# Optimization experiments

Hardware: AMD Instinct MI355X
Metric: run time of the kernel (lower is better)

## Reference

```python
import jax, jax.numpy as jnp
import numpy as np

EPS = 0.97  # ContrastLoss eps
T = 0.07    # temperature

def _embed(x, W, b):
    # Linear + L2 normalize (Normalize(power=2))
    h = x @ W.T + b                     # [B, feat_dim]
    norm = jnp.sqrt(jnp.sum(h * h, axis=1, keepdims=True))
    return h / norm

def setup_inputs() -> dict:
    key = jax.random.key(0)
    ks = jax.random.split(key, 7)
    B, S, Td, F = 8192, 2048, 2048, 128
    return {
        "f_s": jax.random.normal(ks[0], (B, S), jnp.float32),
        "f_t": jax.random.normal(ks[1], (B, Td), jnp.float32),
        "y": jax.random.randint(ks[2], (B,), 0, 100, jnp.int64),
        "W_s": jax.random.normal(ks[3], (F, S), jnp.float32) * 0.02,
        "b_s": jax.random.normal(ks[4], (F,), jnp.float32) * 0.02,
        "W_t": jax.random.normal(ks[5], (F, Td), jnp.float32) * 0.02,
        "b_t": jax.random.normal(ks[6], (F,), jnp.float32) * 0.02,
    }

def reference(f_s, f_t, y, W_s, b_s, W_t, b_t):
    fs = _embed(f_s, W_s, b_s)
    ft = _embed(f_t, W_t, b_t)
    # CRDLoss re-normalizes (idempotent, kept for fidelity)
    fs = fs / jnp.linalg.norm(fs, axis=1, keepdims=True)
    ft = ft / jnp.linalg.norm(ft, axis=1, keepdims=True)
    bsz = fs.shape[0]
    x = jnp.exp((fs @ ft.T) / T)  # [B, B] exponentiated similarities
    same = y[None, :] == y[:, None]        # y_expand == y_expand.T
    diag = jnp.eye(bsz, dtype=bool)
    pos_mask = same & ~diag
    neg_mask = ~same & ~diag
    # masked log-ratio sums instead of dynamic-shape gathers
    log_D1 = jnp.log(x / (x + EPS))
    log_D0 = jnp.log(EPS / (x + EPS))
    loss = -(jnp.sum(jnp.where(pos_mask, log_D1, 0.0))
             + jnp.sum(jnp.where(neg_mask, log_D0, 0.0))) / bsz
    return loss
```

## Files before the change

### kernel.cpp

```cpp
#include <hip/hip_runtime.h>
#include <math.h>


typedef _Float16 half_t;
typedef half_t halfx4 __attribute__((ext_vector_type(4)));
typedef half_t halfx8 __attribute__((ext_vector_type(8)));
typedef float f32x4 __attribute__((ext_vector_type(4)));

#define B_TOT   8192
#define K_EMB   2048
#define F_DIM   128
#define INV_T   14.285714285714286f
#define EPS_C   0.97f
#define LOG_EPS (-0.030459207485f)

__global__ __launch_bounds__(256) void cvt_w_kernel(
    const float* __restrict__ Ws, const float* __restrict__ Wt,
    half_t* __restrict__ Ws16, half_t* __restrict__ Wt16)
{
    const float* src = blockIdx.y ? Wt : Ws;
    half_t* dst = blockIdx.y ? Wt16 : Ws16;
    int pos4 = blockIdx.x * 256 + threadIdx.x;
    float4 v = *(const float4*)(src + (size_t)pos4 * 4);
    halfx4 h4 = {(half_t)v.x, (half_t)v.y, (half_t)v.z, (half_t)v.w};
    *(halfx4*)(dst + (size_t)pos4 * 4) = h4;
}

__global__ __launch_bounds__(256) void embed_kernel(
    const float* __restrict__ Xs, const float* __restrict__ Xt,
    const half_t* __restrict__ Ws16, const half_t* __restrict__ Wt16,
    const float* __restrict__ bs, const float* __restrict__ bt,
    half_t* __restrict__ outs, half_t* __restrict__ outt)
{
    const float* X; const half_t* W16; const float* bias; half_t* out;
    if (blockIdx.y == 0) { X = Xs; W16 = Ws16; bias = bs; out = outs; }
    else                 { X = Xt; W16 = Wt16; bias = bt; out = outt; }

    __shared__ half_t As[2][32][72];
    __shared__ half_t Bs[2][128][72];
    __shared__ float  biasS[128];
    __shared__ float  redS[32][2];
    __shared__ float  invS[32];

    const int tid = threadIdx.x;
    const int r0  = blockIdx.x * 32;
    if (tid < 128) biasS[tid] = bias[tid];

    const int lane = tid & 63;
    const int w    = tid >> 6;
    const int wm   = w & 1, wn = w >> 1;
    const int l16  = lane & 15, lhi = lane >> 4;

    f32x4 acc[4];
    for (int in = 0; in < 4; ++in) acc[in] = f32x4{0.f, 0.f, 0.f, 0.f};

    const int ar0 = tid >> 4, ar1 = (tid + 256) >> 4;
    const int akq = (tid & 15) * 4;
    const int bc  = (tid & 7) * 8;

    float4 na[2]; uint4 nb[4];

    na[0] = *(const float4*)(X + (size_t)(r0 + ar0) * K_EMB + akq);
    na[1] = *(const float4*)(X + (size_t)(r0 + ar1) * K_EMB + akq);
#pragma unroll
    for (int i = 0; i < 4; ++i)
        nb[i] = *(const uint4*)(W16 + (size_t)((tid + i * 256) >> 3) * K_EMB + bc);
    {
        halfx4 h0 = {(half_t)na[0].x, (half_t)na[0].y, (half_t)na[0].z, (half_t)na[0].w};
        halfx4 h1 = {(half_t)na[1].x, (half_t)na[1].y, (half_t)na[1].z, (half_t)na[1].w};
        *(halfx4*)&As[0][ar0][akq] = h0;
        *(halfx4*)&As[0][ar1][akq] = h1;
#pragma unroll
        for (int i = 0; i < 4; ++i)
            *(uint4*)&Bs[0][(tid + i * 256) >> 3][bc] = nb[i];
    }
    __syncthreads();

    for (int it = 0; it < 32; ++it) {
        const int cur = it & 1;
        if (it < 31) {
            const int kb = (it + 1) * 64;
            na[0] = *(const float4*)(X + (size_t)(r0 + ar0) * K_EMB + kb + akq);
            na[1] = *(const float4*)(X + (size_t)(r0 + ar1) * K_EMB + kb + akq);
#pragma unroll
            for (int i = 0; i < 4; ++i)
                nb[i] = *(const uint4*)(W16 + (size_t)((tid + i * 256) >> 3) * K_EMB + kb + bc);
        }
#pragma unroll
        for (int kk = 0; kk < 2; ++kk) {
            halfx8 a, b[4];
            a = *(const halfx8*)&As[cur][wm * 16 + l16][kk * 32 + lhi * 8];
#pragma unroll
            for (int in = 0; in < 4; ++in)
                b[in] = *(const halfx8*)&Bs[cur][wn * 64 + in * 16 + l16][kk * 32 + lhi * 8];
#pragma unroll
            for (int in = 0; in < 4; ++in)
                acc[in] = __builtin_amdgcn_mfma_f32_16x16x32_f16(a, b[in], acc[in], 0, 0, 0);
        }
        if (it < 31) {
            const int nxt = cur ^ 1;
            halfx4 h0 = {(half_t)na[0].x, (half_t)na[0].y, (half_t)na[0].z, (half_t)na[0].w};
            halfx4 h1 = {(half_t)na[1].x, (half_t)na[1].y, (half_t)na[1].z, (half_t)na[1].w};
            *(halfx4*)&As[nxt][ar0][akq] = h0;
            *(halfx4*)&As[nxt][ar1][akq] = h1;
#pragma unroll
            for (int i = 0; i < 4; ++i)
                *(uint4*)&Bs[nxt][(tid + i * 256) >> 3][bc] = nb[i];
        }
        __syncthreads();
    }

    float h[4][4];
    float psum[4];
#pragma unroll
    for (int reg = 0; reg < 4; ++reg) {
        float p = 0.f;
#pragma unroll
        for (int in = 0; in < 4; ++in) {
            int col = wn * 64 + in * 16 + l16;
            float v = acc[in][reg] + biasS[col];
            h[in][reg] = v;
            p += v * v;
        }
        p += __shfl_xor(p, 1);
        p += __shfl_xor(p, 2);
        p += __shfl_xor(p, 4);
        p += __shfl_xor(p, 8);
        psum[reg] = p;
    }
    if (l16 == 0)
#pragma unroll
        for (int reg = 0; reg < 4; ++reg)
            redS[wm * 16 + lhi * 4 + reg][wn] = psum[reg];
    __syncthreads();
    if (tid < 32) invS[tid] = rsqrtf(redS[tid][0] + redS[tid][1]);
    __syncthreads();

#pragma unroll
    for (int in = 0; in < 4; ++in)
#pragma unroll
        for (int reg = 0; reg < 4; ++reg) {
            int row = wm * 16 + lhi * 4 + reg;
            int col = wn * 64 + in * 16 + l16;
            out[(size_t)(r0 + row) * F_DIM + col] = (half_t)(h[in][reg] * invS[row]);
        }
}

__global__ __launch_bounds__(256) void loss_kernel(
    const half_t* __restrict__ FS, const half_t* __restrict__ FT,
    const int* __restrict__ y, double* __restrict__ partials)
{
    __shared__ uint4 As4[128 * 8];
    __shared__ uint4 Bs4[128 * 8];
    __shared__ int   yrl[128], ycl[128];
    __shared__ float wsum[4];

    const int tid = threadIdx.x;
    const int i0  = blockIdx.x * 128;
    const int j0  = blockIdx.y * 128;

    if (tid < 128) yrl[tid] = y[i0 + tid];
    else           ycl[tid - 128] = y[j0 + tid - 128];

    const int lane = tid & 63;
    const int w    = tid >> 6;
    const int wm   = w >> 1, wn = w & 1;
    const int l16  = lane & 15, lhi = lane >> 4;

#pragma unroll
    for (int i = 0; i < 4; ++i) {
        int f = tid + i * 256;
        int row = f >> 3, c = f & 7;
        As4[row * 8 + (c ^ (row & 7))] = *(const uint4*)(FS + (size_t)(i0 + row) * F_DIM + c * 8);
    }
#pragma unroll
    for (int i = 0; i < 4; ++i) {
        int f = tid + i * 256;
        int row = f >> 3, c = f & 7;
        Bs4[row * 8 + (c ^ (row & 7))] = *(const uint4*)(FT + (size_t)(j0 + row) * F_DIM + c * 8);
    }
    __syncthreads();

    f32x4 acc[4][4];
    for (int im = 0; im < 4; ++im)
        for (int in = 0; in < 4; ++in)
            acc[im][in] = f32x4{0.f, 0.f, 0.f, 0.f};

    for (int kc = 0; kc < 2; ++kc) {
#pragma unroll
        for (int kk = 0; kk < 2; ++kk) {
            halfx8 a[4], b[4];
#pragma unroll
            for (int im = 0; im < 4; ++im) {
                int r = wm * 64 + im * 16 + l16;
                a[im] = *(const halfx8*)&As4[r * 8 + ((kk * 4 + lhi) ^ (r & 7))];
            }
#pragma unroll
            for (int in = 0; in < 4; ++in) {
                int r = wn * 64 + in * 16 + l16;
                b[in] = *(const halfx8*)&Bs4[r * 8 + ((kk * 4 + lhi) ^ (r & 7))];
            }
#pragma unroll
            for (int im = 0; im < 4; ++im)
#pragma unroll
                for (int in = 0; in < 4; ++in)
                    acc[im][in] = __builtin_amdgcn_mfma_f32_16x16x32_f16(
                        a[im], b[in], acc[im][in], 0, 0, 0);
        }
        if (kc == 0) {
            __syncthreads();
#pragma unroll
            for (int i = 0; i < 4; ++i) {
                int f = tid + i * 256;
                int row = f >> 3, c = f & 7;
                As4[row * 8 + (c ^ (row & 7))] =
                    *(const uint4*)(FS + (size_t)(i0 + row) * F_DIM + 64 + c * 8);
            }
#pragma unroll
            for (int i = 0; i < 4; ++i) {
                int f = tid + i * 256;
                int row = f >> 3, c = f & 7;
                Bs4[row * 8 + (c ^ (row & 7))] =
                    *(const uint4*)(FT + (size_t)(j0 + row) * F_DIM + 64 + c * 8);
            }
            __syncthreads();
        }
    }

    float local = 0.f;
    for (int im = 0; im < 4; ++im) {
        for (int reg = 0; reg < 4; ++reg) {
            int il = wm * 64 + im * 16 + lhi * 4 + reg;
            int yi = yrl[il];
            int gi = i0 + il;
            for (int in = 0; in < 4; ++in) {
                int jl = wn * 64 + in * 16 + l16;
                float s  = acc[im][in][reg];
                float sT = s * INV_T;
                float e  = __expf(sT);
                float l  = __logf(e + EPS_C);
                float term = (yi == ycl[jl]) ? (sT - l) : (LOG_EPS - l);
                if (gi != (j0 + jl)) local += term;
            }
        }
    }
    for (int m = 1; m < 64; m <<= 1) local += __shfl_xor(local, m);
    if (lane == 0) wsum[w] = local;
    __syncthreads();
    if (tid == 0)
        partials[blockIdx.y * gridDim.x + blockIdx.x] =
            ((double)wsum[0] + (double)wsum[1]) + ((double)wsum[2] + (double)wsum[3]);
}

__global__ __launch_bounds__(256) void finalize_kernel(
    const double* __restrict__ partials, float* __restrict__ out)
{
    __shared__ double sh[4];
    double loc = 0.0;
    for (int i = threadIdx.x; i < 4096; i += 256) loc += partials[i];
    for (int m = 1; m < 64; m <<= 1) loc += __shfl_xor(loc, m);
    int lane = threadIdx.x & 63, w = threadIdx.x >> 6;
    if (lane == 0) sh[w] = loc;
    __syncthreads();
    if (threadIdx.x == 0)
        out[0] = (float)(-(sh[0] + sh[1] + sh[2] + sh[3]) / (double)B_TOT);
}

extern "C" void kernel_launch(void* const* d_in, const int* in_sizes, int n_in,
                              void* d_out, int out_size, void* d_ws, size_t ws_size,
                              hipStream_t stream)
{
    const size_t WS_NEEDED = (64 << 10) + (4 << 20) + (1 << 20);
    if (ws_size < WS_NEEDED) return;

    const float* f_s = (const float*)d_in[0];
    const float* f_t = (const float*)d_in[1];
    const int*   y   = (const int*)d_in[2];
    const float* W_s = (const float*)d_in[3];
    const float* b_s = (const float*)d_in[4];
    const float* W_t = (const float*)d_in[5];
    const float* b_t = (const float*)d_in[6];
    float* out = (float*)d_out;

    char* ws = (char*)d_ws;
    double* partials = (double*)ws;
    half_t* fs   = (half_t*)(ws + (64 << 10));
    half_t* ft   = (half_t*)(ws + (64 << 10) + (2 << 20));
    half_t* Ws16 = (half_t*)(ws + (64 << 10) + (4 << 20));
    half_t* Wt16 = (half_t*)(ws + (64 << 10) + (4 << 20) + (512 << 10));

    cvt_w_kernel<<<dim3(256, 2), 256, 0, stream>>>(W_s, W_t, Ws16, Wt16);
    embed_kernel<<<dim3(256, 2), 256, 0, stream>>>(f_s, f_t, Ws16, Wt16, b_s, b_t, fs, ft);
    loss_kernel<<<dim3(64, 64), 256, 0, stream>>>(fs, ft, y, partials);
    finalize_kernel<<<1, 256, 0, stream>>>(partials, out);
    (void)in_sizes; (void)n_in; (void)out_size;
}
```

Measured before the change: 215.2 us.

## Retile embed GEMM to 16-row blocks with XOR-swizzled LDS and staggered K order

The embedding GEMM now uses 16-row blocks (1024 blocks instead of 512) and a 128-wide K step. Each wave covers 32 output columns across all 16 rows. LDS tiles switch to an XOR-swizzled uint4 layout in place of padding, and odd blocks start at a different K offset so concurrent blocks spread their W reads. This aims to raise occupancy and parallelism for the memory-bound embedding pass, at the cost of reloading W more often per output row.

```diff
diff --git a/kernel.cpp b/kernel.cpp
--- a/kernel.cpp
+++ b/kernel.cpp
@@ -36,88 +36,97 @@
     if (blockIdx.y == 0) { X = Xs; W16 = Ws16; bias = bs; out = outs; }
     else                 { X = Xt; W16 = Wt16; bias = bt; out = outt; }
 
-    __shared__ half_t As[2][32][72];
-    __shared__ half_t Bs[2][128][72];
-    __shared__ float  biasS[128];
-    __shared__ float  redS[32][2];
-    __shared__ float  invS[32];
+    __shared__ uint4 As4[2][16 * 16];
+    __shared__ uint4 Bs4[2][128 * 16];
+    __shared__ float biasS[128];
+    __shared__ float redS[16][4];
+    __shared__ float invS[16];
 
     const int tid = threadIdx.x;
-    const int r0  = blockIdx.x * 32;
+    const int r0  = blockIdx.x * 16;
     if (tid < 128) biasS[tid] = bias[tid];
 
     const int lane = tid & 63;
     const int w    = tid >> 6;
-    const int wm   = w & 1, wn = w >> 1;
     const int l16  = lane & 15, lhi = lane >> 4;
 
-    f32x4 acc[4];
-    for (int in = 0; in < 4; ++in) acc[in] = f32x4{0.f, 0.f, 0.f, 0.f};
-
-    const int ar0 = tid >> 4, ar1 = (tid + 256) >> 4;
-    const int akq = (tid & 15) * 4;
-    const int bc  = (tid & 7) * 8;
-
-    float4 na[2]; uint4 nb[4];
-
-    na[0] = *(const float4*)(X + (size_t)(r0 + ar0) * K_EMB + akq);
-    na[1] = *(const float4*)(X + (size_t)(r0 + ar1) * K_EMB + akq);
-#pragma unroll
-    for (int i = 0; i < 4; ++i)
-        nb[i] = *(const uint4*)(W16 + (size_t)((tid + i * 256) >> 3) * K_EMB + bc);
+    const int ph = (blockIdx.x & 1) * 8;
+
+    f32x4 acc[2];
+    acc[0] = f32x4{0.f, 0.f, 0.f, 0.f};
+    acc[1] = f32x4{0.f, 0.f, 0.f, 0.f};
+
+    const int arow = tid >> 4, ac = tid & 15;
+
+    float4 na0, na1; uint4 nb[8];
+
     {
-        halfx4 h0 = {(half_t)na[0].x, (half_t)na[0].y, (half_t)na[0].z, (half_t)na[0].w};
-        halfx4 h1 = {(half_t)na[1].x, (half_t)na[1].y, (half_t)na[1].z, (half_t)na[1].w};
-        *(halfx4*)&As[0][ar0][akq] = h0;
-        *(halfx4*)&As[0][ar1][akq] = h1;
-#pragma unroll
-        for (int i = 0; i < 4; ++i)
-            *(uint4*)&Bs[0][(tid + i * 256) >> 3][bc] = nb[i];
-    }
-    __syncthreads();
-
-    for (int it = 0; it < 32; ++it) {
+        const int kb = ph * 128;
+        na0 = *(const float4*)(X + (size_t)(r0 + arow) * K_EMB + kb + ac * 8);
+        na1 = *(const float4*)(X + (size_t)(r0 + arow) * K_EMB + kb + ac * 8 + 4);
+#pragma unroll
+        for (int i = 0; i < 8; ++i) {
+            int g = tid + i * 256;
+            nb[i] = *(const uint4*)(W16 + (size_t)(g >> 4) * K_EMB + kb + (g & 15) * 8);
+        }
+        halfx8 h8 = {(half_t)na0.x, (half_t)na0.y, (half_t)na0.z, (half_t)na0.w,
+                     (half_t)na1.x, (half_t)na1.y, (half_t)na1.z, (half_t)na1.w};
+        *(halfx8*)&As4[0][arow * 16 + (ac ^ arow)] = h8;
+#pragma unroll
+        for (int i = 0; i < 8; ++i) {
+            int g = tid + i * 256;
+            Bs4[0][(g >> 4) * 16 + ((g & 15) ^ ((g >> 4) & 15))] = nb[i];
+        }
+    }
+    __syncthreads();
+
+    for (int it = 0; it < 16; ++it) {
         const int cur = it & 1;
-        if (it < 31) {
-            const int kb = (it + 1) * 64;
-            na[0] = *(const float4*)(X + (size_t)(r0 + ar0) * K_EMB + kb + akq);
-            na[1] = *(const float4*)(X + (size_t)(r0 + ar1) * K_EMB + kb + akq);
-#pragma unroll
-            for (int i = 0; i < 4; ++i)
-                nb[i] = *(const uint4*)(W16 + (size_t)((tid + i * 256) >> 3) * K_EMB + kb + bc);
-        }
-#pragma unroll
-        for (int kk = 0; kk < 2; ++kk) {
-            halfx8 a, b[4];
-            a = *(const halfx8*)&As[cur][wm * 16 + l16][kk * 32 + lhi * 8];
-#pragma unroll
-            for (int in = 0; in < 4; ++in)
-                b[in] = *(const halfx8*)&Bs[cur][wn * 64 + in * 16 + l16][kk * 32 + lhi * 8];
-#pragma unroll
-            for (int in = 0; in < 4; ++in)
+        if (it < 15) {
+            const int kb = (((it + 1 + ph) & 15)) * 128;
+            na0 = *(const float4*)(X + (size_t)(r0 + arow) * K_EMB + kb + ac * 8);
+            na1 = *(const float4*)(X + (size_t)(r0 + arow) * K_EMB + kb + ac * 8 + 4);
+#pragma unroll
+            for (int i = 0; i < 8; ++i) {
+                int g = tid + i * 256;
+                nb[i] = *(const uint4*)(W16 + (size_t)(g >> 4) * K_EMB + kb + (g & 15) * 8);
+            }
+        }
+#pragma unroll
+        for (int kk = 0; kk < 4; ++kk) {
+            halfx8 a, b[2];
+            a = *(const halfx8*)&As4[cur][l16 * 16 + ((kk * 4 + lhi) ^ l16)];
+#pragma unroll
+            for (int in = 0; in < 2; ++in) {
+                int r = w * 32 + in * 16 + l16;
+                b[in] = *(const halfx8*)&Bs4[cur][r * 16 + ((kk * 4 + lhi) ^ l16)];
+            }
+#pragma unroll
+            for (int in = 0; in < 2; ++in)
                 acc[in] = __builtin_amdgcn_mfma_f32_16x16x32_f16(a, b[in], acc[in], 0, 0, 0);
         }
-        if (it < 31) {
+        if (it < 15) {
             const int nxt = cur ^ 1;
-            halfx4 h0 = {(half_t)na[0].x, (half_t)na[0].y, (half_t)na[0].z, (half_t)na[0].w};
-            halfx4 h1 = {(half_t)na[1].x, (half_t)na[1].y, (half_t)na[1].z, (half_t)na[1].w};
-            *(halfx4*)&As[nxt][ar0][akq] = h0;
-            *(halfx4*)&As[nxt][ar1][akq] = h1;
-#pragma unroll
-            for (int i = 0; i < 4; ++i)
-                *(uint4*)&Bs[nxt][(tid + i * 256) >> 3][bc] = nb[i];
+            halfx8 h8 = {(half_t)na0.x, (half_t)na0.y, (half_t)na0.z, (half_t)na0.w,
+                         (half_t)na1.x, (half_t)na1.y, (half_t)na1.z, (half_t)na1.w};
+            *(halfx8*)&As4[nxt][arow * 16 + (ac ^ arow)] = h8;
+#pragma unroll
+            for (int i = 0; i < 8; ++i) {
+                int g = tid + i * 256;
+                Bs4[nxt][(g >> 4) * 16 + ((g & 15) ^ ((g >> 4) & 15))] = nb[i];
+            }
         }
         __syncthreads();
     }
 
-    float h[4][4];
+    float h[2][4];
     float psum[4];
 #pragma unroll
     for (int reg = 0; reg < 4; ++reg) {
         float p = 0.f;
 #pragma unroll
-        for (int in = 0; in < 4; ++in) {
-            int col = wn * 64 + in * 16 + l16;
+        for (int in = 0; in < 2; ++in) {
+            int col = w * 32 + in * 16 + l16;
             float v = acc[in][reg] + biasS[col];
             h[in][reg] = v;
             p += v * v;
@@ -131,17 +140,18 @@
     if (l16 == 0)
 #pragma unroll
         for (int reg = 0; reg < 4; ++reg)
-            redS[wm * 16 + lhi * 4 + reg][wn] = psum[reg];
-    __syncthreads();
-    if (tid < 32) invS[tid] = rsqrtf(redS[tid][0] + redS[tid][1]);
-    __syncthreads();
-
-#pragma unroll
-    for (int in = 0; in < 4; ++in)
+            redS[lhi * 4 + reg][w] = psum[reg];
+    __syncthreads();
+    if (tid < 16)
+        invS[tid] = rsqrtf(redS[tid][0] + redS[tid][1] + redS[tid][2] + redS[tid][3]);
+    __syncthreads();
+
+#pragma unroll
+    for (int in = 0; in < 2; ++in)
 #pragma unroll
         for (int reg = 0; reg < 4; ++reg) {
-            int row = wm * 16 + lhi * 4 + reg;
-            int col = wn * 64 + in * 16 + l16;
+            int row = lhi * 4 + reg;
+            int col = w * 32 + in * 16 + l16;
             out[(size_t)(r0 + row) * F_DIM + col] = (half_t)(h[in][reg] * invS[row]);
         }
 }
@@ -290,7 +300,7 @@
     half_t* Wt16 = (half_t*)(ws + (64 << 10) + (4 << 20) + (512 << 10));
 
     cvt_w_kernel<<<dim3(256, 2), 256, 0, stream>>>(W_s, W_t, Ws16, Wt16);
-    embed_kernel<<<dim3(256, 2), 256, 0, stream>>>(f_s, f_t, Ws16, Wt16, b_s, b_t, fs, ft);
+    embed_kernel<<<dim3(512, 2), 256, 0, stream>>>(f_s, f_t, Ws16, Wt16, b_s, b_t, fs, ft);
     loss_kernel<<<dim3(64, 64), 256, 0, stream>>>(fs, ft, y, partials);
     finalize_kernel<<<1, 256, 0, stream>>>(partials, out);
     (void)in_sizes; (void)n_in; (void)out_size;
```

After: 223.5 us. 1.04x slower.
